# Kernel optimization log

Hardware: AMD Instinct MI355X
Metric: run time of the kernel (lower is better)

## Reference

```python
import jax, jax.numpy as jnp
import numpy as np

NQ = 4
NL = 3
# Z-expectation sign table: state axis order = wire order, reshape(-1) => wire 0 is MSB
_bits = (np.arange(2 ** NQ)[:, None] >> np.arange(NQ - 1, -1, -1)) & 1
Z_SIGNS = jnp.asarray((1 - 2 * _bits).astype(np.float32))  # (16, 4)
_CNOT = jnp.asarray(np.array([[1, 0, 0, 0], [0, 1, 0, 0], [0, 0, 0, 1], [0, 0, 1, 0]],
                             dtype=np.complex64).reshape(2, 2, 2, 2))


def _rx(t):
    c = jnp.cos(t / 2).astype(jnp.complex64)
    s = (-1j) * jnp.sin(t / 2).astype(jnp.complex64)
    return jnp.stack([jnp.stack([c, s]), jnp.stack([s, c])])


def _rot(phi, theta, omega):
    # PennyLane Rot = RZ(omega) @ RY(theta) @ RZ(phi)
    ez = jnp.exp(-0.5j * phi.astype(jnp.complex64))
    zero = jnp.zeros_like(ez)
    rz1 = jnp.stack([jnp.stack([ez, zero]), jnp.stack([zero, jnp.conj(ez)])])
    c = jnp.cos(theta / 2).astype(jnp.complex64)
    s = jnp.sin(theta / 2).astype(jnp.complex64)
    ry = jnp.stack([jnp.stack([c, -s]), jnp.stack([s, c])])
    eo = jnp.exp(-0.5j * omega.astype(jnp.complex64))
    rz2 = jnp.stack([jnp.stack([eo, zero]), jnp.stack([zero, jnp.conj(eo)])])
    return rz2 @ ry @ rz1


def _apply1(state, U, wire):
    state = jnp.tensordot(U, state, axes=[[1], [wire]])
    return jnp.moveaxis(state, 0, wire)


def _apply_cnot(state, c, t):
    state = jnp.tensordot(_CNOT, state, axes=[[2, 3], [c, t]])
    return jnp.moveaxis(state, [0, 1], [c, t])


def _circuit(x4, qw):
    state = jnp.zeros((2,) * NQ, jnp.complex64).at[(0,) * NQ].set(1.0)
    for i in range(NQ):
        state = _apply1(state, _rx(x4[i]), i)
    for layer in range(NL):
        for q in range(NQ):
            state = _apply1(state, _rot(qw[layer, q, 0], qw[layer, q, 1], qw[layer, q, 2]), q)
        for q in range(NQ - 1):
            state = _apply_cnot(state, q, q + 1)
    probs = jnp.abs(state.reshape(-1)) ** 2  # (16,)
    return probs @ Z_SIGNS  # (NQ,) PauliZ expectations


def setup_inputs() -> dict:
    key = jax.random.key(0)
    ks = jax.random.split(key, 16)
    D, H1, H2, L = 2048, 128, 64, 32
    B = 16384
    s = 0.02
    return {
        "x": jax.random.normal(ks[0], (B, D), jnp.float32),
        "enc_w0": jax.random.normal(ks[1], (D, H1), jnp.float32) * s,
        "enc_b0": jnp.zeros((H1,), jnp.float32),
        "enc_w1": jax.random.normal(ks[2], (H1, H2), jnp.float32) * s,
        "enc_b1": jnp.zeros((H2,), jnp.float32),
        "enc_w2": jax.random.normal(ks[3], (H2, L), jnp.float32) * s,
        "enc_b2": jnp.zeros((L,), jnp.float32),
        "qw": jax.random.normal(ks[4], (NL, NQ, 3), jnp.float32),
        "dec_w0": jax.random.normal(ks[5], (NQ, H2), jnp.float32) * s,
        "dec_b0": jnp.zeros((H2,), jnp.float32),
        "dec_w1": jax.random.normal(ks[6], (H2, H1), jnp.float32) * s,
        "dec_b1": jnp.zeros((H1,), jnp.float32),
        "dec_w2": jax.random.normal(ks[7], (H1, D), jnp.float32) * s,
        "dec_b2": jnp.zeros((D,), jnp.float32),
    }


def reference(x, enc_w0, enc_b0, enc_w1, enc_b1, enc_w2, enc_b2, qw,
              dec_w0, dec_b0, dec_w1, dec_b1, dec_w2, dec_b2):
    # Encoder (eval mode: dropout is identity)
    h = jax.nn.relu(x @ enc_w0 + enc_b0)
    h = jax.nn.relu(h @ enc_w1 + enc_b1)
    latent = h @ enc_w2 + enc_b2  # (B, 32)
    # Quantum refinement: circuit only reads latent[:, :NQ]
    refined = jax.vmap(lambda xi: _circuit(xi, qw))(latent[:, :NQ]).astype(jnp.float32)  # (B, 4)
    # Decoder
    h = jax.nn.relu(refined @ dec_w0 + dec_b0)
    h = jax.nn.relu(h @ dec_w1 + dec_b1)
    return h @ dec_w2 + dec_b2
```

## Files before the change

### kernel.cpp

```cpp
#include <hip/hip_runtime.h>
#include <hip/hip_bf16.h>

typedef __attribute__((ext_vector_type(8))) short short8;
typedef __attribute__((ext_vector_type(4))) float f32x4;

#define DEVI __device__ __forceinline__

DEVI unsigned short f2bf(float f) {
    union { float f; unsigned u; } v; v.f = f;
    unsigned r = v.u + 0x7FFFu + ((v.u >> 16) & 1u);
    return (unsigned short)(r >> 16);
}

DEVI unsigned cvtpk_bf16(float lo, float hi) {
    float2 t; t.x = lo; t.y = hi;
    __hip_bfloat162 h = __float22bfloat162_rn(t);
    union { __hip_bfloat162 h; unsigned u; } c; c.h = h;
    return c.u;
}

DEVI void gload_lds16(const void* g, void* l) {
    __builtin_amdgcn_global_load_lds(
        (const __attribute__((address_space(1))) unsigned int*)(unsigned long long)g,
        (__attribute__((address_space(3))) unsigned int*)(unsigned int)(unsigned long long)l,
        16, 0, 0);
}

DEVI void run_circuit(const float lat[4], const float* __restrict__ qw, float out4[4])
{
    float cw[4], sw[4];
#pragma unroll
    for (int w = 0; w < 4; ++w) sincosf(0.5f * lat[w], &sw[w], &cw[w]);

    float sr[16], si[16];
#pragma unroll
    for (int s = 0; s < 16; ++s) {
        float mag = 1.f; int p = 0;
#pragma unroll
        for (int w = 0; w < 4; ++w) {
            int b = (s >> (3 - w)) & 1;
            mag *= b ? sw[w] : cw[w];
            p += b;
        }
        p &= 3;
        sr[s] = (p == 0) ? mag : ((p == 2) ? -mag : 0.f);
        si[s] = (p == 1) ? -mag : ((p == 3) ? mag : 0.f);
    }

#pragma unroll
    for (int L = 0; L < 3; ++L) {
#pragma unroll
        for (int q = 0; q < 4; ++q) {
            const float* gq = qw + (L * 4 + q) * 3;
            float phi = gq[0], th = gq[1], om = gq[2];
            float ct, st;
            sincosf(0.5f * th, &st, &ct);
            float ap = 0.5f * (phi + om), am = 0.5f * (phi - om);
            float cap, sap, cam, sam;
            sincosf(ap, &sap, &cap);
            sincosf(am, &sam, &cam);
            float u00r =  ct * cap, u00i = -ct * sap;
            float u01r = -st * cam, u01i = -st * sam;
            float u10r =  st * cam, u10i = -st * sam;
            float u11r =  ct * cap, u11i =  ct * sap;
            int bm = 8 >> q;
#pragma unroll
            for (int i = 0; i < 16; ++i) {
                if (i & bm) continue;
                int j = i | bm;
                float ar = sr[i], ai = si[i], br = sr[j], bi = si[j];
                sr[i] = u00r*ar - u00i*ai + u01r*br - u01i*bi;
                si[i] = u00r*ai + u00i*ar + u01r*bi + u01i*br;
                sr[j] = u10r*ar - u10i*ai + u11r*br - u11i*bi;
                si[j] = u10r*ai + u10i*ar + u11r*bi + u11i*br;
            }
        }
#pragma unroll
        for (int q = 0; q < 3; ++q) {
            int cm = 8 >> q, tm = 8 >> (q + 1);
#pragma unroll
            for (int i = 0; i < 16; ++i) {
                if ((i & cm) && !(i & tm)) {
                    int j = i | tm;
                    float tr = sr[i]; sr[i] = sr[j]; sr[j] = tr;
                    float ti = si[i]; si[i] = si[j]; si[j] = ti;
                }
            }
        }
    }
#pragma unroll
    for (int q = 0; q < 4; ++q) {
        int bm = 8 >> q;
        float e = 0.f;
#pragma unroll
        for (int i = 0; i < 16; ++i) {
            float p = sr[i]*sr[i] + si[i]*si[i];
            e += (i & bm) ? -p : p;
        }
        out4[q] = e;
    }
}

__global__ void prep_kernel(const float* __restrict__ ew0, const float* __restrict__ ew1,
                            const float* __restrict__ dw1, const float* __restrict__ dw2,
                            unsigned short* __restrict__ wsb)
{
    int i = blockIdx.x * 256 + threadIdx.x;
    if (i < 262144) {
        int n = i >> 11, k = i & 2047;
        wsb[i] = f2bf(ew0[k * 128 + n]);
    } else if (i < 270336) {
        int t = i - 262144; int n = t >> 7, k = t & 127;
        wsb[i] = f2bf(ew1[k * 64 + n]);
    } else if (i < 278528) {
        int t = i - 270336; int n = t >> 6, k = t & 63;
        wsb[i] = f2bf(dw1[k * 128 + n]);
    } else if (i < 540672) {
        int t = i - 278528; int n = t >> 7, k = t & 127;
        wsb[i] = f2bf(dw2[k * 2048 + n]);
    }
}

__launch_bounds__(256, 2)
__global__ void fused_kernel(const float* __restrict__ x,
                             const unsigned short* __restrict__ w0T,
                             const float* __restrict__ b0e,
                             const unsigned short* __restrict__ w1eT,
                             const float* __restrict__ b1e,
                             const float* __restrict__ w2e,
                             const float* __restrict__ b2e,
                             const float* __restrict__ qw,
                             const float* __restrict__ w0d,
                             const float* __restrict__ b0d,
                             const unsigned short* __restrict__ w1dT,
                             const float* __restrict__ b1d,
                             const unsigned short* __restrict__ w2T,
                             const float* __restrict__ b2d,
                             float* __restrict__ out)
{
    __shared__ __align__(16) char smem[81920];
    char* const H1   = smem + 49152;
    float* const H2  = (float*)(smem + 57344);
    float* const W2C = (float*)(smem + 65664);
    float* const W0D = (float*)(smem + 66688);
    float* const B0D = (float*)(smem + 67712);
    char* const HD   = smem + 68096;
    char* const GA   = smem + 72192;
    char* const W1E  = smem;
    char* const W1D  = smem + 16384;

    const int tid = threadIdx.x;
    const int lane = tid & 63;
    const int wv = tid >> 6;
    const int wm = wv >> 1, wn = wv & 1;
    const int l16 = lane & 15, lq = lane >> 4;
    const int m0 = blockIdx.x * 32;

    {
        const int rA0 = wv * 8 + (lane >> 4);
        const int rA1 = wv * 8 + 4 + (lane >> 4);
        const int slA0 = (lane & 15) ^ ((rA0 & 7) << 1);
        const int slA1 = (lane & 15) ^ ((rA1 & 7) << 1);
        const char* sA0 = (const char*)(x + (long)(m0 + rA0) * 2048 + slA0 * 4);
        const char* sA1 = (const char*)(x + (long)(m0 + rA1) * 2048 + slA1 * 4);
        const int rB0 = wv * 32 +  0 + (lane >> 3);
        const int rB1 = wv * 32 +  8 + (lane >> 3);
        const int rB2 = wv * 32 + 16 + (lane >> 3);
        const int rB3 = wv * 32 + 24 + (lane >> 3);
        const char* sB0 = (const char*)(w0T + rB0 * 2048 + ((lane & 7) ^ (rB0 & 7)) * 8);
        const char* sB1 = (const char*)(w0T + rB1 * 2048 + ((lane & 7) ^ (rB1 & 7)) * 8);
        const char* sB2 = (const char*)(w0T + rB2 * 2048 + ((lane & 7) ^ (rB2 & 7)) * 8);
        const char* sB3 = (const char*)(w0T + rB3 * 2048 + ((lane & 7) ^ (rB3 & 7)) * 8);
        const int aoff0 = wv * 2048;
        const int aoff1 = wv * 2048 + 1024;
        const int boff0 = wv * 4096;
        const int boff1 = wv * 4096 + 1024;
        const int boff2 = wv * 4096 + 2048;
        const int boff3 = wv * 4096 + 3072;

        auto issue = [&](int cur) {
            char* Ab = smem + (cur ? 8192 : 0);
            char* Bb = smem + (cur ? 32768 : 16384);
            gload_lds16(sA0, Ab + aoff0); sA0 += 256;
            gload_lds16(sA1, Ab + aoff1); sA1 += 256;
            gload_lds16(sB0, Bb + boff0); sB0 += 128;
            gload_lds16(sB1, Bb + boff1); sB1 += 128;
            gload_lds16(sB2, Bb + boff2); sB2 += 128;
            gload_lds16(sB3, Bb + boff3); sB3 += 128;
        };

        f32x4 acc[4];
#pragma unroll
        for (int b = 0; b < 4; ++b) acc[b] = (f32x4)(0.f);

        const int arow = wm * 16 + l16;
        const unsigned aswz = (unsigned)((arow & 7) << 1);

        issue(0);
        __syncthreads();

        for (int t = 0; t < 32; ++t) {
            if (t < 31) issue((t + 1) & 1);
            const char* Ab = smem + ((t & 1) ? 8192 : 0);
            const char* Bb = smem + ((t & 1) ? 32768 : 16384);
#pragma unroll
            for (int kk = 0; kk < 2; ++kk) {
                const int c = kk * 8 + lq * 2;
                const char* ap = Ab + arow * 256 + (((unsigned)c ^ aswz) << 4);
                float4 f0 = *(const float4*)ap;
                float4 f1 = *(const float4*)(ap + 16);
                union { unsigned u[4]; short8 s; } pk;
                pk.u[0] = cvtpk_bf16(f0.x, f0.y);
                pk.u[1] = cvtpk_bf16(f0.z, f0.w);
                pk.u[2] = cvtpk_bf16(f1.x, f1.y);
                pk.u[3] = cvtpk_bf16(f1.z, f1.w);
                short8 aF = pk.s;
#pragma unroll
                for (int fn = 0; fn < 4; ++fn) {
                    int n = wn * 64 + fn * 16 + l16;
                    short8 bF = *(const short8*)(Bb + n * 128 + (((kk * 4 + lq) ^ (n & 7)) << 4));
                    acc[fn] = __builtin_amdgcn_mfma_f32_16x16x32_bf16(aF, bF, acc[fn], 0, 0, 0);
                }
            }
            __syncthreads();
        }

        {
            const int r16 = wv * 16 + (lane >> 4);
            const int s16 = lane & 15;
            const int r8  = wv * 32 + (lane >> 3);
            const int s8  = lane & 7;
#pragma unroll
            for (int i = 0; i < 4; ++i) {
                int row = r16 + i * 4;
                gload_lds16(w1eT + row * 128 + ((s16 ^ (row & 7)) * 8),
                            W1E + wv * 4096 + i * 1024);
            }
#pragma unroll
            for (int i = 0; i < 4; ++i) {
                int row = r8 + i * 8;
                gload_lds16(w1dT + row * 64 + ((s8 ^ (row & 7)) * 8),
                            W1D + wv * 4096 + i * 1024);
            }
        }
        W2C[tid] = w2e[(tid >> 2) * 32 + (tid & 3)];
        W0D[tid] = w0d[tid];
        if (tid < 64) B0D[tid] = b0d[tid];

        float b0v[4];
#pragma unroll
        for (int fn = 0; fn < 4; ++fn) b0v[fn] = b0e[wn * 64 + fn * 16 + l16];
#pragma unroll
        for (int fn = 0; fn < 4; ++fn)
#pragma unroll
            for (int r = 0; r < 4; ++r) {
                int row = wm * 16 + lq * 4 + r;
                int col = wn * 64 + fn * 16 + l16;
                float v = fmaxf(acc[fn][r] + b0v[fn], 0.f);
                *(unsigned short*)(H1 + row * 256 + ((((col >> 3) ^ (row & 7)) << 4) | ((col & 7) << 1))) = f2bf(v);
            }
    }
    __syncthreads();

    {
        f32x4 acc2[2];
#pragma unroll
        for (int b = 0; b < 2; ++b) acc2[b] = (f32x4)(0.f);
#pragma unroll
        for (int kk = 0; kk < 4; ++kk) {
            int row = wm * 16 + l16;
            short8 aF = *(const short8*)(H1 + row * 256 + (((kk * 4 + lq) ^ (row & 7)) << 4));
#pragma unroll
            for (int fn = 0; fn < 2; ++fn) {
                int n = wn * 32 + fn * 16 + l16;
                short8 bF = *(const short8*)(W1E + n * 256 + (((kk * 4 + lq) ^ (n & 7)) << 4));
                acc2[fn] = __builtin_amdgcn_mfma_f32_16x16x32_bf16(aF, bF, acc2[fn], 0, 0, 0);
            }
        }
        float b1v[2];
#pragma unroll
        for (int fn = 0; fn < 2; ++fn) b1v[fn] = b1e[wn * 32 + fn * 16 + l16];
#pragma unroll
        for (int fn = 0; fn < 2; ++fn)
#pragma unroll
            for (int r = 0; r < 4; ++r) {
                int row = wm * 16 + lq * 4 + r;
                int col = wn * 32 + fn * 16 + l16;
                H2[row * 65 + col] = fmaxf(acc2[fn][r] + b1v[fn], 0.f);
            }
    }
    __syncthreads();

    if (tid < 32) {
        float lat[4];
#pragma unroll
        for (int j = 0; j < 4; ++j) lat[j] = b2e[j];
        const float* h2row = H2 + tid * 65;
#pragma unroll 8
        for (int k = 0; k < 64; ++k) {
            float hv = h2row[k];
#pragma unroll
            for (int j = 0; j < 4; ++j) lat[j] = fmaf(hv, W2C[k * 4 + j], lat[j]);
        }
        float o4[4];
        run_circuit(lat, qw, o4);
#pragma unroll
        for (int s = 0; s < 8; ++s) {
            uint4 pk;
            unsigned tmp[4];
#pragma unroll
            for (int p = 0; p < 4; ++p) {
                int c0 = s * 8 + p * 2;
                float v0 = fmaxf(o4[0]*W0D[c0]     + o4[1]*W0D[64+c0]   + o4[2]*W0D[128+c0]   + o4[3]*W0D[192+c0]   + B0D[c0],   0.f);
                float v1 = fmaxf(o4[0]*W0D[c0+1]   + o4[1]*W0D[64+c0+1] + o4[2]*W0D[128+c0+1] + o4[3]*W0D[192+c0+1] + B0D[c0+1], 0.f);
                tmp[p] = (unsigned)f2bf(v0) | ((unsigned)f2bf(v1) << 16);
            }
            pk.x = tmp[0]; pk.y = tmp[1]; pk.z = tmp[2]; pk.w = tmp[3];
            *(uint4*)(HD + tid * 128 + ((s ^ (tid & 7)) << 4)) = pk;
        }
    }
    __syncthreads();

    {
        f32x4 accg[4];
#pragma unroll
        for (int b = 0; b < 4; ++b) accg[b] = (f32x4)(0.f);
#pragma unroll
        for (int kk = 0; kk < 2; ++kk) {
            int row = wm * 16 + l16;
            short8 aF = *(const short8*)(HD + row * 128 + (((kk * 4 + lq) ^ (row & 7)) << 4));
#pragma unroll
            for (int fn = 0; fn < 4; ++fn) {
                int n = wn * 64 + fn * 16 + l16;
                short8 bF = *(const short8*)(W1D + n * 128 + (((kk * 4 + lq) ^ (n & 7)) << 4));
                accg[fn] = __builtin_amdgcn_mfma_f32_16x16x32_bf16(aF, bF, accg[fn], 0, 0, 0);
            }
        }
        float b1v[4];
#pragma unroll
        for (int fn = 0; fn < 4; ++fn) b1v[fn] = b1d[wn * 64 + fn * 16 + l16];
#pragma unroll
        for (int fn = 0; fn < 4; ++fn)
#pragma unroll
            for (int r = 0; r < 4; ++r) {
                int row = wm * 16 + lq * 4 + r;
                int col = wn * 64 + fn * 16 + l16;
                float v = fmaxf(accg[fn][r] + b1v[fn], 0.f);
                *(unsigned short*)(GA + row * 256 + ((((col >> 3) ^ (row & 7)) << 4) | ((col & 7) << 1))) = f2bf(v);
            }
    }
    __syncthreads();

    {
        auto w2issue = [&](int c) {
            char* W = smem + ((c & 1) ? 16384 : 0);
            int base = c * 64;
#pragma unroll
            for (int i = 0; i < 4; ++i) {
                int row = wv * 16 + i * 4 + (lane >> 4);
                gload_lds16(w2T + (base + row) * 128 + (((lane & 15) ^ (row & 7)) * 8),
                            W + wv * 4096 + i * 1024);
            }
        };
        w2issue(0);
        __syncthreads();

        const int arow = wm * 16 + l16;
        for (int c = 0; c < 32; ++c) {
            if (c < 31) w2issue(c + 1);
            const char* W = smem + ((c & 1) ? 16384 : 0);
            f32x4 a3[2];
#pragma unroll
            for (int b = 0; b < 2; ++b) a3[b] = (f32x4)(0.f);
#pragma unroll
            for (int kk = 0; kk < 4; ++kk) {
                short8 aF = *(const short8*)(GA + arow * 256 + (((kk * 4 + lq) ^ (arow & 7)) << 4));
#pragma unroll
                for (int fn = 0; fn < 2; ++fn) {
                    int n = wn * 32 + fn * 16 + l16;
                    short8 bF = *(const short8*)(W + n * 256 + (((kk * 4 + lq) ^ (n & 7)) << 4));
                    a3[fn] = __builtin_amdgcn_mfma_f32_16x16x32_bf16(aF, bF, a3[fn], 0, 0, 0);
                }
            }
            int n0 = c * 64;
            float b2v[2];
#pragma unroll
            for (int fn = 0; fn < 2; ++fn) b2v[fn] = b2d[n0 + wn * 32 + fn * 16 + l16];
#pragma unroll
            for (int fn = 0; fn < 2; ++fn)
#pragma unroll
                for (int r = 0; r < 4; ++r) {
                    int row = m0 + wm * 16 + lq * 4 + r;
                    int col = n0 + wn * 32 + fn * 16 + l16;
                    out[(long)row * 2048 + col] = a3[fn][r] + b2v[fn];
                }
            __syncthreads();
        }
    }
}

extern "C" void kernel_launch(void* const* d_in, const int* in_sizes, int n_in,
                              void* d_out, int out_size, void* d_ws, size_t ws_size,
                              hipStream_t stream)
{
    (void)in_sizes; (void)n_in; (void)out_size; (void)ws_size;
    const float* x      = (const float*)d_in[0];
    const float* enc_w0 = (const float*)d_in[1];
    const float* enc_b0 = (const float*)d_in[2];
    const float* enc_w1 = (const float*)d_in[3];
    const float* enc_b1 = (const float*)d_in[4];
    const float* enc_w2 = (const float*)d_in[5];
    const float* enc_b2 = (const float*)d_in[6];
    const float* qw     = (const float*)d_in[7];
    const float* dec_w0 = (const float*)d_in[8];
    const float* dec_b0 = (const float*)d_in[9];
    const float* dec_w1 = (const float*)d_in[10];
    const float* dec_b1 = (const float*)d_in[11];
    const float* dec_w2 = (const float*)d_in[12];
    const float* dec_b2 = (const float*)d_in[13];

    unsigned short* wsb = (unsigned short*)d_ws;

    prep_kernel<<<2112, 256, 0, stream>>>(enc_w0, enc_w1, dec_w1, dec_w2, wsb);
    fused_kernel<<<512, 256, 0, stream>>>(x, wsb, enc_b0,
                                          wsb + 262144, enc_b1, enc_w2, enc_b2, qw,
                                          dec_w0, dec_b0, wsb + 270336, dec_b1,
                                          wsb + 278528, dec_b2, (float*)d_out);
}
```

Baseline: 91.56 us.

## Shrink shared memory footprint to fit three blocks per CU

Shared memory drops from 80KB to about 52KB by aliasing H1 and GA and removing the LDS staging of the small decoder and latent weights, which are now read straight from global memory. Launch bounds are raised to three blocks per CU for more occupancy and better latency hiding in the memory-bound first GEMM. The x-tile swizzle is changed to a 16-byte granularity XOR, and output stores become nontemporal to keep the output stream from polluting the cache. The cost is tighter register limits that could cause spills, plus extra global loads in the single-wave circuit stage.

```diff
diff --git a/kernel.cpp b/kernel.cpp
--- a/kernel.cpp
+++ b/kernel.cpp
@@ -121,7 +121,7 @@
     }
 }
 
-__launch_bounds__(256, 2)
+__launch_bounds__(256, 3)
 __global__ void fused_kernel(const float* __restrict__ x,
                              const unsigned short* __restrict__ w0T,
                              const float* __restrict__ b0e,
@@ -138,16 +138,13 @@
                              const float* __restrict__ b2d,
                              float* __restrict__ out)
 {
-    __shared__ __align__(16) char smem[81920];
-    char* const H1   = smem + 49152;
-    float* const H2  = (float*)(smem + 57344);
-    float* const W2C = (float*)(smem + 65664);
-    float* const W0D = (float*)(smem + 66688);
-    float* const B0D = (float*)(smem + 67712);
-    char* const HD   = smem + 68096;
-    char* const GA   = smem + 72192;
+    __shared__ __align__(16) char smem[53376];
     char* const W1E  = smem;
     char* const W1D  = smem + 16384;
+    char* const H1   = smem + 32768;
+    char* const GA   = smem + 32768;
+    float* const H2  = (float*)(smem + 40960);
+    char* const HD   = smem + 49280;
 
     const int tid = threadIdx.x;
     const int lane = tid & 63;
@@ -158,11 +155,9 @@
 
     {
         const int rA0 = wv * 8 + (lane >> 4);
-        const int rA1 = wv * 8 + 4 + (lane >> 4);
-        const int slA0 = (lane & 15) ^ ((rA0 & 7) << 1);
-        const int slA1 = (lane & 15) ^ ((rA1 & 7) << 1);
-        const char* sA0 = (const char*)(x + (long)(m0 + rA0) * 2048 + slA0 * 4);
-        const char* sA1 = (const char*)(x + (long)(m0 + rA1) * 2048 + slA1 * 4);
+        const int rA1 = rA0 + 4;
+        const char* sA0 = (const char*)(x + (long)(m0 + rA0) * 2048 + ((lane & 15) ^ (rA0 & 7)) * 4);
+        const char* sA1 = (const char*)(x + (long)(m0 + rA1) * 2048 + ((lane & 15) ^ (rA1 & 7)) * 4);
         const int rB0 = wv * 32 +  0 + (lane >> 3);
         const int rB1 = wv * 32 +  8 + (lane >> 3);
         const int rB2 = wv * 32 + 16 + (lane >> 3);
@@ -194,7 +189,7 @@
         for (int b = 0; b < 4; ++b) acc[b] = (f32x4)(0.f);
 
         const int arow = wm * 16 + l16;
-        const unsigned aswz = (unsigned)((arow & 7) << 1);
+        const int ah = arow & 7;
 
         issue(0);
         __syncthreads();
@@ -203,12 +198,12 @@
             if (t < 31) issue((t + 1) & 1);
             const char* Ab = smem + ((t & 1) ? 8192 : 0);
             const char* Bb = smem + ((t & 1) ? 32768 : 16384);
+            const char* abase = Ab + arow * 256;
 #pragma unroll
             for (int kk = 0; kk < 2; ++kk) {
                 const int c = kk * 8 + lq * 2;
-                const char* ap = Ab + arow * 256 + (((unsigned)c ^ aswz) << 4);
-                float4 f0 = *(const float4*)ap;
-                float4 f1 = *(const float4*)(ap + 16);
+                float4 f0 = *(const float4*)(abase + ((c ^ ah) << 4));
+                float4 f1 = *(const float4*)(abase + (((c + 1) ^ ah) << 4));
                 union { unsigned u[4]; short8 s; } pk;
                 pk.u[0] = cvtpk_bf16(f0.x, f0.y);
                 pk.u[1] = cvtpk_bf16(f0.z, f0.w);
@@ -243,9 +238,6 @@
                             W1D + wv * 4096 + i * 1024);
             }
         }
-        W2C[tid] = w2e[(tid >> 2) * 32 + (tid & 3)];
-        W0D[tid] = w0d[tid];
-        if (tid < 64) B0D[tid] = b0d[tid];
 
         float b0v[4];
 #pragma unroll
@@ -299,8 +291,11 @@
 #pragma unroll 8
         for (int k = 0; k < 64; ++k) {
             float hv = h2row[k];
-#pragma unroll
-            for (int j = 0; j < 4; ++j) lat[j] = fmaf(hv, W2C[k * 4 + j], lat[j]);
+            float4 wv4 = *(const float4*)(w2e + k * 32);
+            lat[0] = fmaf(hv, wv4.x, lat[0]);
+            lat[1] = fmaf(hv, wv4.y, lat[1]);
+            lat[2] = fmaf(hv, wv4.z, lat[2]);
+            lat[3] = fmaf(hv, wv4.w, lat[3]);
         }
         float o4[4];
         run_circuit(lat, qw, o4);
@@ -311,8 +306,8 @@
 #pragma unroll
             for (int p = 0; p < 4; ++p) {
                 int c0 = s * 8 + p * 2;
-                float v0 = fmaxf(o4[0]*W0D[c0]     + o4[1]*W0D[64+c0]   + o4[2]*W0D[128+c0]   + o4[3]*W0D[192+c0]   + B0D[c0],   0.f);
-                float v1 = fmaxf(o4[0]*W0D[c0+1]   + o4[1]*W0D[64+c0+1] + o4[2]*W0D[128+c0+1] + o4[3]*W0D[192+c0+1] + B0D[c0+1], 0.f);
+                float v0 = fmaxf(o4[0]*w0d[c0]     + o4[1]*w0d[64+c0]   + o4[2]*w0d[128+c0]   + o4[3]*w0d[192+c0]   + b0d[c0],   0.f);
+                float v1 = fmaxf(o4[0]*w0d[c0+1]   + o4[1]*w0d[64+c0+1] + o4[2]*w0d[128+c0+1] + o4[3]*w0d[192+c0+1] + b0d[c0+1], 0.f);
                 tmp[p] = (unsigned)f2bf(v0) | ((unsigned)f2bf(v1) << 16);
             }
             pk.x = tmp[0]; pk.y = tmp[1]; pk.z = tmp[2]; pk.w = tmp[3];
@@ -392,7 +387,7 @@
                 for (int r = 0; r < 4; ++r) {
                     int row = m0 + wm * 16 + lq * 4 + r;
                     int col = n0 + wn * 32 + fn * 16 + l16;
-                    out[(long)row * 2048 + col] = a3[fn][r] + b2v[fn];
+                    __builtin_nontemporal_store(a3[fn][r] + b2v[fn], &out[(long)row * 2048 + col]);
                 }
             __syncthreads();
         }
```

Result: slower. 105.1 us (+14.8%).
